# Performance work log

Measured on AMD Instinct MI355X. Metric: run time of the kernel, lower is better.

## Reference

```python
import jax, jax.numpy as jnp
import numpy as np

B, S, D = 16, 2048, 2048  # S == D required for m_q + output broadcast in original code


def setup_inputs() -> dict:
    key = jax.random.key(0)
    ks = jax.random.split(key, 8)
    scale = 1.0 / np.sqrt(D)
    return {
        "hidden_list": jax.random.normal(ks[0], (B, S, D), dtype=jnp.float32),
        "m_q": jax.random.normal(ks[1], (D,), dtype=jnp.float32),
        "Wq": jax.random.normal(ks[2], (D, D), dtype=jnp.float32) * scale,
        "bq": jax.random.normal(ks[3], (D,), dtype=jnp.float32) * scale,
        "Wm": jax.random.normal(ks[4], (D, D), dtype=jnp.float32) * scale,
        "bm": jax.random.normal(ks[5], (D,), dtype=jnp.float32) * scale,
        "Wa": jax.random.normal(ks[6], (D, D), dtype=jnp.float32) * scale,
        "ba": jax.random.normal(ks[7], (D,), dtype=jnp.float32) * scale,
    }


def reference(hidden_list, m_q, Wq, bq, Wm, bm, Wa, ba):
    # hidden_list: [B, S, D]; m_q: [D]
    hq = jnp.tanh(jnp.einsum("bsd,ed->bse", hidden_list, Wq) + bq)      # [B,S,D]
    mq = jnp.tanh(Wm @ m_q + bm)                                        # [D]
    Sg = hq * mq                                                        # gated bilinear, [B,S,D]
    alpha = jax.nn.softmax(jnp.einsum("bsd,ed->bse", Sg, Wa) + ba, axis=-1)  # [B,S,D]
    output = jnp.sum(alpha * hidden_list, axis=-1)                      # [B,S]
    m_q_new = m_q + output                                              # broadcast [D]+[B,S] (S==D)
    return output, m_q_new
```

## Files before the change

### kernel.cpp

```cpp
#include <hip/hip_runtime.h>

typedef unsigned short u16;
typedef short bf16x8 __attribute__((ext_vector_type(8)));
typedef u16 u16x8 __attribute__((ext_vector_type(8)));
typedef float f32x4 __attribute__((ext_vector_type(4)));

__device__ __forceinline__ float bf2f(u16 u) {
    union { unsigned u; float f; } c; c.u = ((unsigned)u) << 16; return c.f;
}
__device__ __forceinline__ u16 f2bf(float f) {
    union { float f; unsigned u; } c; c.f = f;
    unsigned r = c.u + 0x7FFFu + ((c.u >> 16) & 1u);
    return (u16)(r >> 16);
}
__device__ __forceinline__ float tanh_fast(float x) {
    float e = __expf(2.0f * x);
    return 1.0f - 2.0f / (e + 1.0f);
}
__device__ __forceinline__ void gll16(const void* g, void* l) {
    __builtin_amdgcn_global_load_lds((const __attribute__((address_space(1))) void*)g,
                                     (__attribute__((address_space(3))) void*)l, 16, 0, 0);
}

#define BAR() __builtin_amdgcn_s_barrier()

__global__ __launch_bounds__(256) void cvt_f32_bf16(const float* __restrict__ src,
                                                    u16* __restrict__ dst, int n8) {
    int i = blockIdx.x * blockDim.x + threadIdx.x;
    int stride = gridDim.x * blockDim.x;
    for (; i < n8; i += stride) {
        const float4* s = (const float4*)(src + (size_t)i * 8);
        float4 a = s[0], b = s[1];
        u16x8 o;
        o[0] = f2bf(a.x); o[1] = f2bf(a.y); o[2] = f2bf(a.z); o[3] = f2bf(a.w);
        o[4] = f2bf(b.x); o[5] = f2bf(b.y); o[6] = f2bf(b.z); o[7] = f2bf(b.w);
        *(u16x8*)(dst + (size_t)i * 8) = o;
    }
}

__global__ __launch_bounds__(256) void mq_kernel(const float* __restrict__ Wm,
                                                 const float* __restrict__ q,
                                                 const float* __restrict__ bm,
                                                 float* __restrict__ mq, int D) {
    int w = threadIdx.x >> 6, l = threadIdx.x & 63;
    int e = blockIdx.x * 4 + w;
    const float* wp = Wm + (size_t)e * D;
    float s = 0.f;
    for (int j = 0; j < D; j += 256) {
        float4 wv = *(const float4*)(wp + j + l * 4);
        float4 qv = *(const float4*)(q + j + l * 4);
        s += wv.x * qv.x + wv.y * qv.y + wv.z * qv.z + wv.w * qv.w;
    }
    #pragma unroll
    for (int o = 32; o >= 1; o >>= 1) s += __shfl_xor(s, o);
    if (l == 0) mq[e] = tanh_fast(s + bm[e]);
}

template <int EPI>
__global__ __launch_bounds__(512, 2) void gemm_1b(const u16* __restrict__ A,
                                                  const u16* __restrict__ B,
                                                  const float* __restrict__ bias,
                                                  const float* __restrict__ gate,
                                                  u16* __restrict__ C,
                                                  int M, int N, int K) {
    __shared__ u16 sh[65536];
    char* LDS = (char*)sh;
    const int K2 = K * 2;
    const int KT = K >> 5;

    const int tid = threadIdx.x;
    const int w = tid >> 6, l = tid & 63;
    const int wm = w >> 2, wn = w & 3;

    int orig = blockIdx.x + gridDim.x * blockIdx.y;
    int nwg = gridDim.x * gridDim.y;
    int id = ((nwg & 7) == 0) ? ((orig & 7) * (nwg >> 3) + (orig >> 3)) : orig;
    const int tileN = (id % gridDim.x) * 256;
    const int tileM = (id / gridDim.x) * 256;

    const int e_sw = (l & 7) ^ (l >> 3);
    const int r_lane = 2 * (l >> 3) + (e_sw >> 2);
    const int c_lane = (e_sw & 3) << 4;
    const int ch0 = w * 2, ch1 = w * 2 + 1;
    const char* sA0 = (const char*)A + (size_t)(tileM + ch0 * 16 + r_lane) * K2 + c_lane;
    const char* sA1 = (const char*)A + (size_t)(tileM + ch1 * 16 + r_lane) * K2 + c_lane;
    const char* sB0 = (const char*)B + (size_t)(tileN + ch0 * 16 + r_lane) * K2 + c_lane;
    const char* sB1 = (const char*)B + (size_t)(tileN + ch1 * 16 + r_lane) * K2 + c_lane;
    char* dA0 = LDS + ch0 * 1024;
    char* dA1 = LDS + ch1 * 1024;
    char* dB0 = LDS + 65536 + ch0 * 1024;
    char* dB1 = LDS + 65536 + ch1 * 1024;

#define STG(tk, SB) do { size_t go = (size_t)(tk) * 64;                         \
    gll16(sA0 + go, dA0 + (SB)); gll16(sA1 + go, dA1 + (SB));                   \
    gll16(sB0 + go, dB0 + (SB)); gll16(sB1 + go, dB1 + (SB)); } while (0)

    const int prd = ((l & 15) >> 1) * 128 +
                    ((((l & 1) << 2) | (l >> 4)) ^ ((l & 15) >> 1)) * 16;
    const char* pRA = LDS + wm * 8192 + prd;
    const char* pRB = LDS + 65536 + wn * 4096 + prd;

    f32x4 acc[8][4] = {};

    STG(0, 0); STG(1, 16384);
    asm volatile("s_waitcnt vmcnt(4)" ::: "memory");
    BAR();

#define ITER(t, P) do {                                                         \
    constexpr int SL = (P) * 16384;                                             \
    constexpr int SN = (((P) + 2) & 3) * 16384;                                 \
    bf16x8 af[8], bf[4];                                                        \
    _Pragma("unroll")                                                           \
    for (int fm = 0; fm < 8; ++fm)                                              \
        af[fm] = *(const bf16x8*)(pRA + SL + fm * 1024);                        \
    _Pragma("unroll")                                                           \
    for (int fn = 0; fn < 4; ++fn)                                              \
        bf[fn] = *(const bf16x8*)(pRB + SL + fn * 1024);                        \
    if ((t) + 2 < KT) STG((t) + 2, SN);                                         \
    __builtin_amdgcn_s_setprio(1);                                              \
    _Pragma("unroll")                                                           \
    for (int fm = 0; fm < 8; ++fm)                                              \
        _Pragma("unroll")                                                       \
        for (int fn = 0; fn < 4; ++fn)                                          \
            acc[fm][fn] = __builtin_amdgcn_mfma_f32_16x16x32_bf16(              \
                af[fm], bf[fn], acc[fm][fn], 0, 0, 0);                          \
    __builtin_amdgcn_s_setprio(0);                                              \
    if ((t) + 2 < KT) asm volatile("s_waitcnt vmcnt(4)" ::: "memory");          \
    else              asm volatile("s_waitcnt vmcnt(0)" ::: "memory");          \
    BAR();                                                                      \
} while (0)

    for (int tt = 0; tt < KT; tt += 4) {
        ITER(tt, 0);
        ITER(tt + 1, 1);
        ITER(tt + 2, 2);
        ITER(tt + 3, 3);
    }
#undef ITER
#undef STG

    const int cr = (l >> 4) * 4;
    const int cl = l & 15;
    #pragma unroll
    for (int fn = 0; fn < 4; ++fn) {
        const int col = tileN + wn * 64 + fn * 16 + cl;
        const float bs = bias[col];
        float gt = 0.f;
        if (EPI == 0) gt = gate[col];
        #pragma unroll
        for (int fm = 0; fm < 8; ++fm)
            #pragma unroll
            for (int r = 0; r < 4; ++r) {
                const int row = tileM + wm * 128 + fm * 16 + cr + r;
                float v = acc[fm][fn][r] + bs;
                if (EPI == 0) v = tanh_fast(v) * gt;
                C[(size_t)row * N + col] = f2bf(v);
            }
    }
}

__global__ __launch_bounds__(256) void softmax_out(const u16* __restrict__ logits,
                                                   const float* __restrict__ hidden,
                                                   const float* __restrict__ m_q,
                                                   float* __restrict__ out,
                                                   int D, int R) {
    const int r = blockIdx.x;
    const int t = threadIdx.x;
    const int w = t >> 6, l = t & 63;
    const u16* lp = logits + (size_t)r * D + t * 8;
    const float* hp = hidden + (size_t)r * D + t * 8;

    bf16x8 lv = *(const bf16x8*)lp;
    float lf[8];
    #pragma unroll
    for (int j = 0; j < 8; ++j) lf[j] = bf2f((u16)lv[j]);
    float4 h0 = *(const float4*)hp;
    float4 h1 = *(const float4*)(hp + 4);
    float hv[8] = {h0.x, h0.y, h0.z, h0.w, h1.x, h1.y, h1.z, h1.w};

    float m = lf[0];
    #pragma unroll
    for (int j = 1; j < 8; ++j) m = fmaxf(m, lf[j]);
    #pragma unroll
    for (int o = 32; o >= 1; o >>= 1) m = fmaxf(m, __shfl_xor(m, o));

    __shared__ float red[8];
    if (l == 0) red[w] = m;
    __syncthreads();
    m = fmaxf(fmaxf(red[0], red[1]), fmaxf(red[2], red[3]));
    __syncthreads();

    float se = 0.f, sh = 0.f;
    #pragma unroll
    for (int j = 0; j < 8; ++j) {
        float e = __expf(lf[j] - m);
        se += e;
        sh += e * hv[j];
    }
    #pragma unroll
    for (int o = 32; o >= 1; o >>= 1) { se += __shfl_xor(se, o); sh += __shfl_xor(sh, o); }
    if (l == 0) { red[w] = se; red[4 + w] = sh; }
    __syncthreads();
    if (t == 0) {
        float SE = red[0] + red[1] + red[2] + red[3];
        float SH = red[4] + red[5] + red[6] + red[7];
        float o = SH / SE;
        out[r] = o;
        out[R + r] = m_q[r & (D - 1)] + o;
    }
}

extern "C" void kernel_launch(void* const* d_in, const int* in_sizes, int n_in,
                              void* d_out, int out_size, void* d_ws, size_t ws_size,
                              hipStream_t stream) {
    const float* hidden = (const float*)d_in[0];
    const float* m_q    = (const float*)d_in[1];
    const float* Wq     = (const float*)d_in[2];
    const float* bq     = (const float*)d_in[3];
    const float* Wm     = (const float*)d_in[4];
    const float* bm     = (const float*)d_in[5];
    const float* Wa     = (const float*)d_in[6];
    const float* ba     = (const float*)d_in[7];
    float* out = (float*)d_out;

    const int D = 2048;
    const int M = 16 * 2048;

    char* ws = (char*)d_ws;
    size_t oH  = 0;
    size_t oS  = oH  + (size_t)M * D * 2;
    size_t oWq = oS  + (size_t)M * D * 2;
    size_t oWa = oWq + (size_t)D * D * 2;
    size_t oMq = oWa + (size_t)D * D * 2;
    size_t need = oMq + (size_t)D * sizeof(float);
    if (ws_size < need) return;

    u16* hbf    = (u16*)(ws + oH);
    u16* Sg     = (u16*)(ws + oS);
    u16* Wqb    = (u16*)(ws + oWq);
    u16* Wab    = (u16*)(ws + oWa);
    float* mq   = (float*)(ws + oMq);
    u16* logits = hbf;

    cvt_f32_bf16<<<4096, 256, 0, stream>>>(hidden, hbf, M * D / 8);
    cvt_f32_bf16<<<1024, 256, 0, stream>>>(Wq, Wqb, D * D / 8);
    cvt_f32_bf16<<<1024, 256, 0, stream>>>(Wa, Wab, D * D / 8);
    mq_kernel<<<D / 4, 256, 0, stream>>>(Wm, m_q, bm, mq, D);

    dim3 grid(D / 256, M / 256);
    gemm_1b<0><<<grid, 512, 0, stream>>>(hbf, Wqb, bq, mq, Sg, M, D, D);
    gemm_1b<1><<<grid, 512, 0, stream>>>(Sg, Wab, ba, nullptr, logits, M, D, D);

    softmax_out<<<M, 256, 0, stream>>>(logits, hidden, m_q, out, D, M);
}
```

Before: 692.1 us.

## Switch bf16 GEMMs to 128x128 tiles with 4 waves and double-buffered LDS

Replaces the 256x256-tile, 8-wave GEMM, which used 4-stage LDS buffering of 128 KB, with a 128x128-tile, 4-wave kernel that uses 32 KB of LDS double-buffered. Each wave now computes a 64x64 sub-tile, and the global-to-LDS staging and swizzle are reworked to match. An extra barrier after the LDS reads is needed so the buffer can be reused. The aim is higher occupancy and more workgroups across the CUs. The cost is lower arithmetic intensity per tile, more global traffic, and an additional barrier every K step.

```diff
diff --git a/kernel.cpp b/kernel.cpp
--- a/kernel.cpp
+++ b/kernel.cpp
@@ -57,84 +57,78 @@
 }
 
 template <int EPI>
-__global__ __launch_bounds__(512, 2) void gemm_1b(const u16* __restrict__ A,
+__global__ __launch_bounds__(256, 4) void gemm_hi(const u16* __restrict__ A,
                                                   const u16* __restrict__ B,
                                                   const float* __restrict__ bias,
                                                   const float* __restrict__ gate,
                                                   u16* __restrict__ C,
                                                   int M, int N, int K) {
-    __shared__ u16 sh[65536];
+    __shared__ u16 sh[16384];
     char* LDS = (char*)sh;
     const int K2 = K * 2;
     const int KT = K >> 5;
 
     const int tid = threadIdx.x;
     const int w = tid >> 6, l = tid & 63;
-    const int wm = w >> 2, wn = w & 3;
+    const int wm = w >> 1, wn = w & 1;
 
     int orig = blockIdx.x + gridDim.x * blockIdx.y;
     int nwg = gridDim.x * gridDim.y;
     int id = ((nwg & 7) == 0) ? ((orig & 7) * (nwg >> 3) + (orig >> 3)) : orig;
-    const int tileN = (id % gridDim.x) * 256;
-    const int tileM = (id / gridDim.x) * 256;
-
-    const int e_sw = (l & 7) ^ (l >> 3);
-    const int r_lane = 2 * (l >> 3) + (e_sw >> 2);
-    const int c_lane = (e_sw & 3) << 4;
-    const int ch0 = w * 2, ch1 = w * 2 + 1;
-    const char* sA0 = (const char*)A + (size_t)(tileM + ch0 * 16 + r_lane) * K2 + c_lane;
-    const char* sA1 = (const char*)A + (size_t)(tileM + ch1 * 16 + r_lane) * K2 + c_lane;
-    const char* sB0 = (const char*)B + (size_t)(tileN + ch0 * 16 + r_lane) * K2 + c_lane;
-    const char* sB1 = (const char*)B + (size_t)(tileN + ch1 * 16 + r_lane) * K2 + c_lane;
-    char* dA0 = LDS + ch0 * 1024;
-    char* dA1 = LDS + ch1 * 1024;
-    char* dB0 = LDS + 65536 + ch0 * 1024;
-    char* dB1 = LDS + 65536 + ch1 * 1024;
-
-#define STG(tk, SB) do { size_t go = (size_t)(tk) * 64;                         \
-    gll16(sA0 + go, dA0 + (SB)); gll16(sA1 + go, dA1 + (SB));                   \
-    gll16(sB0 + go, dB0 + (SB)); gll16(sB1 + go, dB1 + (SB)); } while (0)
-
-    const int prd = ((l & 15) >> 1) * 128 +
-                    ((((l & 1) << 2) | (l >> 4)) ^ ((l & 15) >> 1)) * 16;
-    const char* pRA = LDS + wm * 8192 + prd;
-    const char* pRB = LDS + 65536 + wn * 4096 + prd;
-
-    f32x4 acc[8][4] = {};
-
-    STG(0, 0); STG(1, 16384);
+    const int tileN = (id % gridDim.x) * 128;
+    const int tileM = (id / gridDim.x) * 128;
+
+    const int srow = w * 16 + (l >> 2);
+    const int cc = ((l & 3) ^ ((l >> 3) & 3)) << 4;
+    const char* sAr = (const char*)A + (size_t)(tileM + srow) * K2 + cc;
+    const char* sBr = (const char*)B + (size_t)(tileN + srow) * K2 + cc;
+    char* dA = LDS + w * 1024;
+    char* dB = LDS + 16384 + w * 1024;
+    const size_t rowStep = (size_t)64 * K2;
+
+#define STG(tk) do { size_t go = (size_t)(tk) * 64; int sb = ((tk) & 1) * 8192;  \
+    gll16(sAr + go, dA + sb);  gll16(sAr + go + rowStep, dA + sb + 4096);        \
+    gll16(sBr + go, dB + sb);  gll16(sBr + go + rowStep, dB + sb + 4096); } while (0)
+
+    const int rloc = l & 15;
+    const int ph = ((l >> 4) ^ ((rloc >> 1) & 3)) << 4;
+    const char* pA = LDS + (wm * 64 + rloc) * 64 + ph;
+    const char* pB = LDS + 16384 + (wn * 64 + rloc) * 64 + ph;
+
+    f32x4 acc[4][4] = {};
+
+    STG(0); STG(1);
     asm volatile("s_waitcnt vmcnt(4)" ::: "memory");
     BAR();
 
 #define ITER(t, P) do {                                                         \
-    constexpr int SL = (P) * 16384;                                             \
-    constexpr int SN = (((P) + 2) & 3) * 16384;                                 \
-    bf16x8 af[8], bf[4];                                                        \
+    constexpr int SL = (P) * 8192;                                              \
+    bf16x8 af[4], bf[4];                                                        \
     _Pragma("unroll")                                                           \
-    for (int fm = 0; fm < 8; ++fm)                                              \
-        af[fm] = *(const bf16x8*)(pRA + SL + fm * 1024);                        \
+    for (int fm = 0; fm < 4; ++fm)                                              \
+        af[fm] = *(const bf16x8*)(pA + SL + fm * 1024);                         \
     _Pragma("unroll")                                                           \
     for (int fn = 0; fn < 4; ++fn)                                              \
-        bf[fn] = *(const bf16x8*)(pRB + SL + fn * 1024);                        \
-    if ((t) + 2 < KT) STG((t) + 2, SN);                                         \
+        bf[fn] = *(const bf16x8*)(pB + SL + fn * 1024);                         \
+    asm volatile("s_waitcnt lgkmcnt(0)" ::: "memory");                          \
+    BAR();                                                                      \
+    if ((t) + 2 < KT) STG((t) + 2);                                             \
     __builtin_amdgcn_s_setprio(1);                                              \
     _Pragma("unroll")                                                           \
-    for (int fm = 0; fm < 8; ++fm)                                              \
+    for (int fm = 0; fm < 4; ++fm)                                              \
         _Pragma("unroll")                                                       \
         for (int fn = 0; fn < 4; ++fn)                                          \
             acc[fm][fn] = __builtin_amdgcn_mfma_f32_16x16x32_bf16(              \
                 af[fm], bf[fn], acc[fm][fn], 0, 0, 0);                          \
     __builtin_amdgcn_s_setprio(0);                                              \
-    if ((t) + 2 < KT) asm volatile("s_waitcnt vmcnt(4)" ::: "memory");          \
-    else              asm volatile("s_waitcnt vmcnt(0)" ::: "memory");          \
+    if ((t) + 2 < KT)      asm volatile("s_waitcnt vmcnt(4)" ::: "memory");     \
+    else if ((t) + 1 < KT) asm volatile("s_waitcnt vmcnt(0)" ::: "memory");     \
     BAR();                                                                      \
 } while (0)
 
-    for (int tt = 0; tt < KT; tt += 4) {
+    for (int tt = 0; tt < KT; tt += 2) {
         ITER(tt, 0);
         ITER(tt + 1, 1);
-        ITER(tt + 2, 2);
-        ITER(tt + 3, 3);
     }
 #undef ITER
 #undef STG
@@ -148,10 +142,10 @@
         float gt = 0.f;
         if (EPI == 0) gt = gate[col];
         #pragma unroll
-        for (int fm = 0; fm < 8; ++fm)
+        for (int fm = 0; fm < 4; ++fm)
             #pragma unroll
             for (int r = 0; r < 4; ++r) {
-                const int row = tileM + wm * 128 + fm * 16 + cr + r;
+                const int row = tileM + wm * 64 + fm * 16 + cr + r;
                 float v = acc[fm][fn][r] + bs;
                 if (EPI == 0) v = tanh_fast(v) * gt;
                 C[(size_t)row * N + col] = f2bf(v);
@@ -247,9 +241,9 @@
     cvt_f32_bf16<<<1024, 256, 0, stream>>>(Wa, Wab, D * D / 8);
     mq_kernel<<<D / 4, 256, 0, stream>>>(Wm, m_q, bm, mq, D);
 
-    dim3 grid(D / 256, M / 256);
-    gemm_1b<0><<<grid, 512, 0, stream>>>(hbf, Wqb, bq, mq, Sg, M, D, D);
-    gemm_1b<1><<<grid, 512, 0, stream>>>(Sg, Wab, ba, nullptr, logits, M, D, D);
+    dim3 grid(D / 128, M / 128);
+    gemm_hi<0><<<grid, 256, 0, stream>>>(hbf, Wqb, bq, mq, Sg, M, D, D);
+    gemm_hi<1><<<grid, 256, 0, stream>>>(Sg, Wab, ba, nullptr, logits, M, D, D);
 
     softmax_out<<<M, 256, 0, stream>>>(logits, hidden, m_q, out, D, M);
 }
```

Result: slower. 852.3 us (+23.1%).
